# Performance work log

Measured on AMD Instinct MI355X. Metric: run time of the kernel, lower is better.

Reference implementation:

```python
import jax, jax.numpy as jnp
import numpy as np


def setup_inputs() -> dict:
    key = jax.random.key(0)
    k_x, k_g, k_fc, k_pj = jax.random.split(key, 4)
    B, T, C, H, E = 4, 2048, 1024, 2048, 8
    n_layer = 12
    x = jax.random.normal(k_x, (B, T, C), dtype=jnp.float32)
    w_gate = 0.02 * jax.random.normal(k_g, (C, E), dtype=jnp.float32)
    w_fc = 0.02 * jax.random.normal(k_fc, (C, H, E), dtype=jnp.float32)
    w_proj = (0.02 * (2 * n_layer) ** -0.5) * jax.random.normal(k_pj, (H, C, E), dtype=jnp.float32)
    return {"x": x, "w_gate": w_gate, "w_fc": w_fc, "w_proj": w_proj, "top_k": 2}


def reference(x, w_gate, w_fc, w_proj, top_k):
    # x: (B,T,C); w_gate: (C,E); w_fc: (C,H,E); w_proj: (H,C,E)
    E = w_gate.shape[-1]
    gate = jnp.einsum('btc,ce->bte', x, w_gate)                  # gating logits
    top_vals, top_idx = jax.lax.top_k(gate, top_k)               # (B,T,K) — raw logits used as combine weights (as in source)
    # Per-expert combine weight: sum_k top_val_k * onehot(idx_k) — zero for unselected experts.
    # This is mathematically identical to gathering the K expert weight slices per token
    # (the source's gather+einsum) but avoids the (B,T,C,H,K) weight blowup.
    onehot = jax.nn.one_hot(top_idx, E, dtype=x.dtype)           # (B,T,K,E)
    w_e = jnp.einsum('btk,btke->bte', top_vals, onehot)          # (B,T,E)
    h = jax.nn.silu(jnp.einsum('btc,che->bthe', x, w_fc))        # (B,T,H,E)
    o = jnp.einsum('bthe,bte,hce->btc', h, w_e, w_proj)          # weighted expert combine
    return o
```

## Files before the change

kernel.cpp:

```cpp
#include <hip/hip_runtime.h>
#include <hip/hip_bf16.h>


#define NTOK 8192
#define CD   1024
#define HD   2048
#define NE   8
#define NSLOT 16384
#define MTILES 20
#define BK   64
#define PACK_BLOCKS 2048

typedef short  short4_t  __attribute__((ext_vector_type(4)));
typedef short  short8_t  __attribute__((ext_vector_type(8)));
typedef __bf16 bf16x8_t  __attribute__((ext_vector_type(8)));
typedef float  f32x4_t   __attribute__((ext_vector_type(4)));

struct FragArg {
  short8_t v;
  __device__ operator short8_t() const { return v; }
  __device__ operator bf16x8_t() const { return __builtin_bit_cast(bf16x8_t, v); }
};

static __device__ __forceinline__ float b2f(unsigned short u) {
  union { float f; unsigned int i; } w; w.i = ((unsigned int)u) << 16; return w.f;
}
static __device__ __forceinline__ unsigned short f2b(float f) {
  unsigned int u = __float_as_uint(f);
  u += 0x7fffu + ((u >> 16) & 1u);
  return (unsigned short)(u >> 16);
}
static __device__ __forceinline__ void gl2lds16(const void* g, void* l) {
  __builtin_amdgcn_global_load_lds((__attribute__((address_space(1))) void*)g,
                                   (__attribute__((address_space(3))) void*)l,
                                   16, 0, 0);
}

static __device__ __forceinline__ void pack_tile(
    const float* __restrict__ in, unsigned short* __restrict__ out,
    int D0, int D1, int b0, int b1, unsigned short* smem, int t)
{
  int d1i = t & 31, d0q = t >> 5;
  #pragma unroll
  for (int r = 0; r < 4; ++r) {
    int d0i = d0q * 4 + r;
    const float* src = in + ((size_t)(b0 + d0i) * D1 + (b1 + d1i)) * NE;
    float4 v0 = *(const float4*)src;
    float4 v1 = *(const float4*)(src + 4);
    unsigned short* dst0 = &smem[d1i * 40 + d0i];
    dst0[0 * 32 * 40] = f2b(v0.x);
    dst0[1 * 32 * 40] = f2b(v0.y);
    dst0[2 * 32 * 40] = f2b(v0.z);
    dst0[3 * 32 * 40] = f2b(v0.w);
    dst0[4 * 32 * 40] = f2b(v1.x);
    dst0[5 * 32 * 40] = f2b(v1.y);
    dst0[6 * 32 * 40] = f2b(v1.z);
    dst0[7 * 32 * 40] = f2b(v1.w);
  }
  __syncthreads();
  int dchunk = t & 3, d1w = (t >> 2) & 31, ehalf = t >> 7;
  #pragma unroll
  for (int p = 0; p < 4; ++p) {
    int e = ehalf + 2 * p;
    short8_t v = *(const short8_t*)&smem[e * 32 * 40 + d1w * 40 + dchunk * 8];
    *(short8_t*)(out + ((size_t)e * D1 + (b1 + d1w)) * D0 + b0 + dchunk * 8) = v;
  }
}

#define GATE_BLOCKS (NTOK / 4)
__global__ __launch_bounds__(256) void prep_kernel(
    const float* __restrict__ x, const float* __restrict__ wg,
    const float* __restrict__ wfc,
    unsigned short* __restrict__ xb, unsigned short* __restrict__ wfcp,
    int* __restrict__ tok_e, float* __restrict__ tok_v,
    int* __restrict__ g_counts)
{
  __shared__ __align__(16) unsigned short lds[NE * 32 * 40];
  __shared__ int hist[NE];
  int t = threadIdx.x;

  if (blockIdx.x < GATE_BLOCKS) {
    if (t < NE) hist[t] = 0;
    __syncthreads();
    int wv = t >> 6, lane = t & 63;
    int tk = blockIdx.x * 4 + wv;
    const float* xr = x + (size_t)tk * CD;
    unsigned short* xbr = xb + (size_t)tk * CD;
    float acc[NE] = {0, 0, 0, 0, 0, 0, 0, 0};
    #pragma unroll
    for (int jj = 0; jj < 4; ++jj) {
      int c0 = (lane + 64 * jj) * 4;
      float4 xv = *(const float4*)(xr + c0);
      short4_t ob;
      ob[0] = (short)f2b(xv.x); ob[1] = (short)f2b(xv.y);
      ob[2] = (short)f2b(xv.z); ob[3] = (short)f2b(xv.w);
      *(short4_t*)(xbr + c0) = ob;
      #pragma unroll
      for (int j = 0; j < 4; ++j) {
        float xf = (j == 0) ? xv.x : (j == 1) ? xv.y : (j == 2) ? xv.z : xv.w;
        const float* wr = wg + (size_t)(c0 + j) * NE;
        float4 w0 = *(const float4*)wr;
        float4 w1 = *(const float4*)(wr + 4);
        acc[0] += xf * w0.x; acc[1] += xf * w0.y;
        acc[2] += xf * w0.z; acc[3] += xf * w0.w;
        acc[4] += xf * w1.x; acc[5] += xf * w1.y;
        acc[6] += xf * w1.z; acc[7] += xf * w1.w;
      }
    }
    #pragma unroll
    for (int off = 32; off >= 1; off >>= 1)
      #pragma unroll
      for (int e = 0; e < NE; ++e) acc[e] += __shfl_down(acc[e], off, 64);
    if (lane == 0) {
      float v1 = -3.0e38f, v2 = -3.0e38f; int i1 = 0, i2 = 1;
      #pragma unroll
      for (int e = 0; e < NE; ++e) {
        float g = acc[e];
        if (g > v1) { v2 = v1; i2 = i1; v1 = g; i1 = e; }
        else if (g > v2) { v2 = g; i2 = e; }
      }
      tok_e[tk * 2] = i1; tok_e[tk * 2 + 1] = i2;
      tok_v[tk * 2] = v1; tok_v[tk * 2 + 1] = v2;
      atomicAdd(&hist[i1], 1); atomicAdd(&hist[i2], 1);
    }
    __syncthreads();
    if (t < NE && hist[t] > 0) atomicAdd(&g_counts[t], hist[t]);
  } else {
    int pid = blockIdx.x - GATE_BLOCKS;
    int bx = pid & 63, by = pid >> 6;
    pack_tile(wfc, wfcp, CD, HD, by * 32, bx * 32, lds, t);
  }
}

__global__ __launch_bounds__(256) void scatter_kernel(
    const int* __restrict__ tok_e, const float* __restrict__ tok_v,
    const int* __restrict__ g_counts, int* __restrict__ g_cursor,
    int* __restrict__ g_base,
    int* __restrict__ bucket_tok, float* __restrict__ bucket_v,
    int* __restrict__ slot_of)
{
  int gid = blockIdx.x * 256 + threadIdx.x;
  int lane = threadIdx.x & 63;
  int base[NE];
  { int o = 0;
    #pragma unroll
    for (int e = 0; e < NE; ++e) { base[e] = o; o += g_counts[e]; } }
  int e = tok_e[gid];
  unsigned long long lanebit = 1ull << lane;
  int pos = 0;
  #pragma unroll
  for (int ee = 0; ee < NE; ++ee) {
    unsigned long long m = __ballot(e == ee);
    if (e == ee) {
      int leader = __ffsll((long long)m) - 1;
      int cnt = __popcll(m);
      int start = 0;
      if (lane == leader) start = atomicAdd(&g_cursor[ee], cnt);
      start = __shfl(start, leader, 64);
      pos = start + __popcll(m & (lanebit - 1));
    }
  }
  int sl = base[e] + pos;
  bucket_tok[sl] = gid >> 1;
  bucket_v[sl]   = tok_v[gid];
  slot_of[gid]   = sl;
  if (gid < NE) g_base[gid] = base[gid];
}

__global__ __launch_bounds__(256) void gemm1_kernel(
    const unsigned short* __restrict__ xb, const unsigned short* __restrict__ wfcp,
    const float* __restrict__ wpj, unsigned short* __restrict__ wpjp,
    const int* __restrict__ g_counts, const int* __restrict__ g_base,
    const int* __restrict__ bucket_tok, const float* __restrict__ bucket_v,
    unsigned short* __restrict__ hbuf)
{
  __shared__ __align__(16) unsigned short smem[128 * BK * 2];
  __shared__ int   s_tok[128];
  __shared__ float s_v[128];
  int t = threadIdx.x;

  if (blockIdx.x < PACK_BLOCKS) {
    int pid = blockIdx.x;
    int bx = pid & 63, by = pid >> 6;
    pack_tile(wpj, wpjp, HD, CD, bx * 32, by * 32, smem, t);
    return;
  }

  int id = blockIdx.x - PACK_BLOCKS;
  int e = id & 7;
  int r = id >> 3;
  int nt = r & 15;
  int mt = r >> 4;

  int cnt = g_counts[e];
  int m0 = mt * 128;
  if (m0 >= cnt) return;
  int base = g_base[e];
  int n0 = nt * 128;

  unsigned short* lsA = smem;
  unsigned short* lsB = smem + 128 * BK;

  if (t < 128) {
    int ok = (m0 + t) < cnt;
    s_tok[t] = ok ? bucket_tok[base + m0 + t] : 0;
    s_v[t]   = ok ? bucket_v[base + m0 + t] : 0.0f;
  }
  __syncthreads();

  int lane = t & 63, wv = t >> 6;
  int subrow = lane >> 3, kc = lane & 7;
  const unsigned short* pA[4]; const unsigned short* pB[4];
  unsigned short* dA[4]; unsigned short* dB[4];
  #pragma unroll
  for (int p = 0; p < 4; ++p) {
    int rr = p * 32 + wv * 8 + subrow;
    int gc = kc ^ ((rr >> 1) & 7);
    pA[p] = xb + (size_t)s_tok[rr] * CD + gc * 8;
    pB[p] = wfcp + ((size_t)e * HD + n0 + rr) * CD + gc * 8;
    dA[p] = &lsA[(p * 32 + wv * 8) * BK];
    dB[p] = &lsB[(p * 32 + wv * 8) * BK];
  }

  int wm = (wv & 1) * 64, wn = (wv >> 1) * 64;
  int ml = lane & 15, kq = lane >> 4;

  f32x4_t acc[4][4];
  #pragma unroll
  for (int i = 0; i < 4; ++i)
    #pragma unroll
    for (int j = 0; j < 4; ++j) acc[i][j] = (f32x4_t){0.f, 0.f, 0.f, 0.f};

  for (int k0 = 0; k0 < CD; k0 += BK) {
    __syncthreads();
    #pragma unroll
    for (int p = 0; p < 4; ++p) {
      gl2lds16(pA[p], dA[p]); pA[p] += BK;
      gl2lds16(pB[p], dB[p]); pB[p] += BK;
    }
    __syncthreads();
    #pragma unroll
    for (int s = 0; s < 2; ++s) {
      short8_t af[4], bfr[4];
      #pragma unroll
      for (int i = 0; i < 4; ++i) {
        int ar = wm + i * 16 + ml;
        af[i]  = *(const short8_t*)&lsA[ar * BK + (((s * 4 + kq) ^ ((ar >> 1) & 7)) * 8)];
        int br = wn + i * 16 + ml;
        bfr[i] = *(const short8_t*)&lsB[br * BK + (((s * 4 + kq) ^ ((br >> 1) & 7)) * 8)];
      }
      #pragma unroll
      for (int i = 0; i < 4; ++i)
        #pragma unroll
        for (int j = 0; j < 4; ++j)
          acc[i][j] = __builtin_amdgcn_mfma_f32_16x16x32_bf16(
              FragArg{af[i]}, FragArg{bfr[j]}, acc[i][j], 0, 0, 0);
    }
  }

  #pragma unroll
  for (int i = 0; i < 4; ++i) {
    int rb = wm + i * 16 + kq * 4;
    #pragma unroll
    for (int r2 = 0; r2 < 4; ++r2) {
      int row = rb + r2;
      if (m0 + row < cnt) {
        float v = s_v[row];
        size_t ro = (size_t)(base + m0 + row) * HD + n0;
        #pragma unroll
        for (int j = 0; j < 4; ++j) {
          float z = acc[i][j][r2];
          float val = v * (z / (1.0f + __expf(-z)));
          hbuf[ro + wn + j * 16 + ml] = f2b(val);
        }
      }
    }
  }
}

__global__ __launch_bounds__(256) void gemm2_kernel(
    const unsigned short* __restrict__ hbuf, const unsigned short* __restrict__ wpjp,
    const int* __restrict__ g_counts, const int* __restrict__ g_base,
    unsigned short* __restrict__ oslot)
{
  int id = blockIdx.x;
  int e = id & 7;
  int r = id >> 3;
  int nt = r & 7;
  int mt = r >> 3;

  int cnt = g_counts[e];
  int m0 = mt * 128;
  if (m0 >= cnt) return;
  int base = g_base[e];
  int n0 = nt * 128;

  __shared__ __align__(16) unsigned short lsA[128 * BK];
  __shared__ __align__(16) unsigned short lsB[128 * BK];

  int t = threadIdx.x;
  int lane = t & 63, wv = t >> 6;
  int subrow = lane >> 3, kc = lane & 7;
  const unsigned short* pA[4]; const unsigned short* pB[4];
  unsigned short* dA[4]; unsigned short* dB[4];
  #pragma unroll
  for (int p = 0; p < 4; ++p) {
    int rr = p * 32 + wv * 8 + subrow;
    int gc = kc ^ ((rr >> 1) & 7);
    pA[p] = hbuf + ((size_t)(base + m0 + rr)) * HD + gc * 8;
    pB[p] = wpjp + ((size_t)e * CD + n0 + rr) * HD + gc * 8;
    dA[p] = &lsA[(p * 32 + wv * 8) * BK];
    dB[p] = &lsB[(p * 32 + wv * 8) * BK];
  }

  int wm = (wv & 1) * 64, wn = (wv >> 1) * 64;
  int ml = lane & 15, kq = lane >> 4;

  f32x4_t acc[4][4];
  #pragma unroll
  for (int i = 0; i < 4; ++i)
    #pragma unroll
    for (int j = 0; j < 4; ++j) acc[i][j] = (f32x4_t){0.f, 0.f, 0.f, 0.f};

  for (int k0 = 0; k0 < HD; k0 += BK) {
    __syncthreads();
    #pragma unroll
    for (int p = 0; p < 4; ++p) {
      gl2lds16(pA[p], dA[p]); pA[p] += BK;
      gl2lds16(pB[p], dB[p]); pB[p] += BK;
    }
    __syncthreads();
    #pragma unroll
    for (int s = 0; s < 2; ++s) {
      short8_t af[4], bfr[4];
      #pragma unroll
      for (int i = 0; i < 4; ++i) {
        int ar = wm + i * 16 + ml;
        af[i]  = *(const short8_t*)&lsA[ar * BK + (((s * 4 + kq) ^ ((ar >> 1) & 7)) * 8)];
        int br = wn + i * 16 + ml;
        bfr[i] = *(const short8_t*)&lsB[br * BK + (((s * 4 + kq) ^ ((br >> 1) & 7)) * 8)];
      }
      #pragma unroll
      for (int i = 0; i < 4; ++i)
        #pragma unroll
        for (int j = 0; j < 4; ++j)
          acc[i][j] = __builtin_amdgcn_mfma_f32_16x16x32_bf16(
              FragArg{af[i]}, FragArg{bfr[j]}, acc[i][j], 0, 0, 0);
    }
  }

  #pragma unroll
  for (int i = 0; i < 4; ++i) {
    int rb = wm + i * 16 + kq * 4;
    #pragma unroll
    for (int r2 = 0; r2 < 4; ++r2) {
      int row = rb + r2;
      if (m0 + row < cnt) {
        size_t ro = (size_t)(base + m0 + row) * CD + n0;
        #pragma unroll
        for (int j = 0; j < 4; ++j)
          oslot[ro + wn + j * 16 + ml] = f2b(acc[i][j][r2]);
      }
    }
  }
}

__global__ __launch_bounds__(256) void combine_kernel(
    const unsigned short* __restrict__ oslot, const int* __restrict__ slot_of,
    float* __restrict__ out)
{
  int gid = blockIdx.x * 256 + threadIdx.x;
  int tk = gid >> 7;
  int ch = (gid & 127) * 8;
  int s0 = slot_of[tk * 2], s1 = slot_of[tk * 2 + 1];
  short8_t a = *(const short8_t*)(oslot + (size_t)s0 * CD + ch);
  short8_t b = *(const short8_t*)(oslot + (size_t)s1 * CD + ch);
  float* op = out + (size_t)tk * CD + ch;
  float4 o0, o1;
  o0.x = b2f((unsigned short)a[0]) + b2f((unsigned short)b[0]);
  o0.y = b2f((unsigned short)a[1]) + b2f((unsigned short)b[1]);
  o0.z = b2f((unsigned short)a[2]) + b2f((unsigned short)b[2]);
  o0.w = b2f((unsigned short)a[3]) + b2f((unsigned short)b[3]);
  o1.x = b2f((unsigned short)a[4]) + b2f((unsigned short)b[4]);
  o1.y = b2f((unsigned short)a[5]) + b2f((unsigned short)b[5]);
  o1.z = b2f((unsigned short)a[6]) + b2f((unsigned short)b[6]);
  o1.w = b2f((unsigned short)a[7]) + b2f((unsigned short)b[7]);
  *(float4*)op = o0;
  *(float4*)(op + 4) = o1;
}

extern "C" void kernel_launch(void* const* d_in, const int* in_sizes, int n_in,
                              void* d_out, int out_size, void* d_ws, size_t ws_size,
                              hipStream_t stream)
{
  const float* x   = (const float*)d_in[0];
  const float* wg  = (const float*)d_in[1];
  const float* wfc = (const float*)d_in[2];
  const float* wpj = (const float*)d_in[3];
  float* out = (float*)d_out;

  char* w = (char*)d_ws;
  unsigned short* wfcp  = (unsigned short*)w; w += (size_t)NE * HD * CD * 2;
  unsigned short* wpjp  = (unsigned short*)w; w += (size_t)NE * CD * HD * 2;
  unsigned short* xb    = (unsigned short*)w; w += (size_t)NTOK * CD * 2;
  unsigned short* hbuf  = (unsigned short*)w; w += (size_t)NSLOT * HD * 2;
  unsigned short* oslot = (unsigned short*)w; w += (size_t)NSLOT * CD * 2;
  int*   tok_e      = (int*)w;   w += NSLOT * 4;
  float* tok_v      = (float*)w; w += NSLOT * 4;
  int*   slot_of    = (int*)w;   w += NSLOT * 4;
  int*   bucket_tok = (int*)w;   w += NSLOT * 4;
  float* bucket_v   = (float*)w; w += NSLOT * 4;
  int*   g_counts   = (int*)w;   w += NE * 4;
  int*   g_cursor   = (int*)w;   w += NE * 4;
  int*   g_base     = (int*)w;   w += 256;

  hipMemsetAsync(g_counts, 0, 2 * NE * sizeof(int), stream);
  prep_kernel<<<GATE_BLOCKS + PACK_BLOCKS, 256, 0, stream>>>(
      x, wg, wfc, xb, wfcp, tok_e, tok_v, g_counts);
  scatter_kernel<<<NSLOT / 256, 256, 0, stream>>>(
      tok_e, tok_v, g_counts, g_cursor, g_base, bucket_tok, bucket_v, slot_of);
  gemm1_kernel<<<PACK_BLOCKS + (HD / 128) * MTILES * NE, 256, 0, stream>>>(
      xb, wfcp, wpj, wpjp, g_counts, g_base, bucket_tok, bucket_v, hbuf);
  gemm2_kernel<<<(CD / 128) * MTILES * NE, 256, 0, stream>>>(
      hbuf, wpjp, g_counts, g_base, oslot);
  combine_kernel<<<(NTOK * CD / 8) / 256, 256, 0, stream>>>(oslot, slot_of, out);
}
```

Before: 449.8 us.

## Double-buffer LDS with half-K staging and explicit waitcnt pipelining in expert GEMMs

Both expert GEMM kernels move from a load, sync, compute loop to a double-buffered LDS pipeline. K tiles are split into 32-wide halves, and global-to-LDS copies for later halves are issued while MFMAs run on the current half. The code uses explicit s_waitcnt vmcnt counts with raw s_barrier calls, raises wave priority around MFMA blocks, and uses a new swizzle for the 32-column layout. Launch bounds now request 2 blocks per CU. The goal is to hide global-load latency behind matrix math, at the cost of hand-counted wait logic that breaks if the number of loads per stage changes.

```diff
diff --git a/kernel.cpp b/kernel.cpp
--- a/kernel.cpp
+++ b/kernel.cpp
@@ -9,6 +9,8 @@
 #define NSLOT 16384
 #define MTILES 20
 #define BK   64
+#define NT1  (CD / BK)
+#define NT2  (HD / BK)
 #define PACK_BLOCKS 2048
 
 typedef short  short4_t  __attribute__((ext_vector_type(4)));
@@ -167,14 +169,14 @@
   if (gid < NE) g_base[gid] = base[gid];
 }
 
-__global__ __launch_bounds__(256) void gemm1_kernel(
+__global__ __launch_bounds__(256, 2) void gemm1_kernel(
     const unsigned short* __restrict__ xb, const unsigned short* __restrict__ wfcp,
     const float* __restrict__ wpj, unsigned short* __restrict__ wpjp,
     const int* __restrict__ g_counts, const int* __restrict__ g_base,
     const int* __restrict__ bucket_tok, const float* __restrict__ bucket_v,
     unsigned short* __restrict__ hbuf)
 {
-  __shared__ __align__(16) unsigned short smem[128 * BK * 2];
+  __shared__ __align__(16) unsigned short smem[2][2][2][128][32];
   __shared__ int   s_tok[128];
   __shared__ float s_v[128];
   int t = threadIdx.x;
@@ -182,7 +184,7 @@
   if (blockIdx.x < PACK_BLOCKS) {
     int pid = blockIdx.x;
     int bx = pid & 63, by = pid >> 6;
-    pack_tile(wpj, wpjp, HD, CD, bx * 32, by * 32, smem, t);
+    pack_tile(wpj, wpjp, HD, CD, bx * 32, by * 32, &smem[0][0][0][0][0], t);
     return;
   }
 
@@ -198,9 +200,6 @@
   int base = g_base[e];
   int n0 = nt * 128;
 
-  unsigned short* lsA = smem;
-  unsigned short* lsB = smem + 128 * BK;
-
   if (t < 128) {
     int ok = (m0 + t) < cnt;
     s_tok[t] = ok ? bucket_tok[base + m0 + t] : 0;
@@ -209,21 +208,26 @@
   __syncthreads();
 
   int lane = t & 63, wv = t >> 6;
-  int subrow = lane >> 3, kc = lane & 7;
-  const unsigned short* pA[4]; const unsigned short* pB[4];
-  unsigned short* dA[4]; unsigned short* dB[4];
-  #pragma unroll
-  for (int p = 0; p < 4; ++p) {
-    int rr = p * 32 + wv * 8 + subrow;
-    int gc = kc ^ ((rr >> 1) & 7);
-    pA[p] = xb + (size_t)s_tok[rr] * CD + gc * 8;
-    pB[p] = wfcp + ((size_t)e * HD + n0 + rr) * CD + gc * 8;
-    dA[p] = &lsA[(p * 32 + wv * 8) * BK];
-    dB[p] = &lsB[(p * 32 + wv * 8) * BK];
-  }
+  int srow = t >> 2;
+  int spc  = t & 3;
+  int sw   = (spc ^ (srow & 3)) * 8;
+  const unsigned short* aS0 = xb + (size_t)s_tok[srow] * CD + sw;
+  const unsigned short* aS1 = xb + (size_t)s_tok[srow + 64] * CD + sw;
+  const unsigned short* bS0 = wfcp + ((size_t)e * HD + n0 + srow) * CD + sw;
+  const unsigned short* bS1 = wfcp + ((size_t)e * HD + n0 + srow + 64) * CD + sw;
+
+  #define STG1(tt, kh) do {                                              \
+    int _ko = (tt) * BK + (kh) * 32;                                     \
+    int _b  = (tt) & 1;                                                  \
+    gl2lds16(aS0 + _ko, &smem[0][_b][kh][wv * 16][0]);                   \
+    gl2lds16(aS1 + _ko, &smem[0][_b][kh][64 + wv * 16][0]);              \
+    gl2lds16(bS0 + _ko, &smem[1][_b][kh][wv * 16][0]);                   \
+    gl2lds16(bS1 + _ko, &smem[1][_b][kh][64 + wv * 16][0]);              \
+  } while (0)
 
   int wm = (wv & 1) * 64, wn = (wv >> 1) * 64;
   int ml = lane & 15, kq = lane >> 4;
+  int sw8 = (kq ^ (ml & 3)) * 8;
 
   f32x4_t acc[4][4];
   #pragma unroll
@@ -231,32 +235,55 @@
     #pragma unroll
     for (int j = 0; j < 4; ++j) acc[i][j] = (f32x4_t){0.f, 0.f, 0.f, 0.f};
 
-  for (int k0 = 0; k0 < CD; k0 += BK) {
-    __syncthreads();
-    #pragma unroll
-    for (int p = 0; p < 4; ++p) {
-      gl2lds16(pA[p], dA[p]); pA[p] += BK;
-      gl2lds16(pB[p], dB[p]); pB[p] += BK;
-    }
-    __syncthreads();
-    #pragma unroll
-    for (int s = 0; s < 2; ++s) {
-      short8_t af[4], bfr[4];
-      #pragma unroll
-      for (int i = 0; i < 4; ++i) {
-        int ar = wm + i * 16 + ml;
-        af[i]  = *(const short8_t*)&lsA[ar * BK + (((s * 4 + kq) ^ ((ar >> 1) & 7)) * 8)];
-        int br = wn + i * 16 + ml;
-        bfr[i] = *(const short8_t*)&lsB[br * BK + (((s * 4 + kq) ^ ((br >> 1) & 7)) * 8)];
-      }
-      #pragma unroll
-      for (int i = 0; i < 4; ++i)
-        #pragma unroll
-        for (int j = 0; j < 4; ++j)
-          acc[i][j] = __builtin_amdgcn_mfma_f32_16x16x32_bf16(
-              FragArg{af[i]}, FragArg{bfr[j]}, acc[i][j], 0, 0, 0);
-    }
-  }
+  STG1(0, 0); STG1(0, 1); STG1(1, 0);
+  asm volatile("s_waitcnt vmcnt(8)" ::: "memory");
+  __builtin_amdgcn_s_barrier();
+  asm volatile("" ::: "memory");
+
+  #pragma unroll 1
+  for (int tt = 0; tt < NT1; ++tt) {
+    int buf = tt & 1;
+    short8_t af[4], bfr[4];
+    #pragma unroll
+    for (int i = 0; i < 4; ++i) {
+      af[i]  = *(const short8_t*)&smem[0][buf][0][wm + i * 16 + ml][sw8];
+      bfr[i] = *(const short8_t*)&smem[1][buf][0][wn + i * 16 + ml][sw8];
+    }
+    if (tt + 1 < NT1) STG1(tt + 1, 1);
+    __builtin_amdgcn_s_barrier();
+    __builtin_amdgcn_s_setprio(1);
+    #pragma unroll
+    for (int i = 0; i < 4; ++i)
+      #pragma unroll
+      for (int j = 0; j < 4; ++j)
+        acc[i][j] = __builtin_amdgcn_mfma_f32_16x16x32_bf16(
+            FragArg{af[i]}, FragArg{bfr[j]}, acc[i][j], 0, 0, 0);
+    __builtin_amdgcn_s_setprio(0);
+    if (tt < NT1 - 1) asm volatile("s_waitcnt vmcnt(8)" ::: "memory");
+    else              asm volatile("s_waitcnt vmcnt(0)" ::: "memory");
+    __builtin_amdgcn_s_barrier();
+    asm volatile("" ::: "memory");
+    #pragma unroll
+    for (int i = 0; i < 4; ++i) {
+      af[i]  = *(const short8_t*)&smem[0][buf][1][wm + i * 16 + ml][sw8];
+      bfr[i] = *(const short8_t*)&smem[1][buf][1][wn + i * 16 + ml][sw8];
+    }
+    if (tt + 2 < NT1) STG1(tt + 2, 0);
+    __builtin_amdgcn_s_barrier();
+    __builtin_amdgcn_s_setprio(1);
+    #pragma unroll
+    for (int i = 0; i < 4; ++i)
+      #pragma unroll
+      for (int j = 0; j < 4; ++j)
+        acc[i][j] = __builtin_amdgcn_mfma_f32_16x16x32_bf16(
+            FragArg{af[i]}, FragArg{bfr[j]}, acc[i][j], 0, 0, 0);
+    __builtin_amdgcn_s_setprio(0);
+    if (tt + 2 < NT1)      asm volatile("s_waitcnt vmcnt(8)" ::: "memory");
+    else if (tt + 1 < NT1) asm volatile("s_waitcnt vmcnt(4)" ::: "memory");
+    __builtin_amdgcn_s_barrier();
+    asm volatile("" ::: "memory");
+  }
+  #undef STG1
 
   #pragma unroll
   for (int i = 0; i < 4; ++i) {
@@ -278,11 +305,13 @@
   }
 }
 
-__global__ __launch_bounds__(256) void gemm2_kernel(
+__global__ __launch_bounds__(256, 2) void gemm2_kernel(
     const unsigned short* __restrict__ hbuf, const unsigned short* __restrict__ wpjp,
     const int* __restrict__ g_counts, const int* __restrict__ g_base,
     unsigned short* __restrict__ oslot)
 {
+  __shared__ __align__(16) unsigned short smem[2][2][2][128][32];
+
   int id = blockIdx.x;
   int e = id & 7;
   int r = id >> 3;
@@ -295,26 +324,28 @@
   int base = g_base[e];
   int n0 = nt * 128;
 
-  __shared__ __align__(16) unsigned short lsA[128 * BK];
-  __shared__ __align__(16) unsigned short lsB[128 * BK];
-
   int t = threadIdx.x;
   int lane = t & 63, wv = t >> 6;
-  int subrow = lane >> 3, kc = lane & 7;
-  const unsigned short* pA[4]; const unsigned short* pB[4];
-  unsigned short* dA[4]; unsigned short* dB[4];
-  #pragma unroll
-  for (int p = 0; p < 4; ++p) {
-    int rr = p * 32 + wv * 8 + subrow;
-    int gc = kc ^ ((rr >> 1) & 7);
-    pA[p] = hbuf + ((size_t)(base + m0 + rr)) * HD + gc * 8;
-    pB[p] = wpjp + ((size_t)e * CD + n0 + rr) * HD + gc * 8;
-    dA[p] = &lsA[(p * 32 + wv * 8) * BK];
-    dB[p] = &lsB[(p * 32 + wv * 8) * BK];
-  }
+  int srow = t >> 2;
+  int spc  = t & 3;
+  int sw   = (spc ^ (srow & 3)) * 8;
+  const unsigned short* aS0 = hbuf + ((size_t)(base + m0 + srow)) * HD + sw;
+  const unsigned short* aS1 = hbuf + ((size_t)(base + m0 + srow + 64)) * HD + sw;
+  const unsigned short* bS0 = wpjp + ((size_t)e * CD + n0 + srow) * HD + sw;
+  const unsigned short* bS1 = wpjp + ((size_t)e * CD + n0 + srow + 64) * HD + sw;
+
+  #define STG2(tt, kh) do {                                              \
+    int _ko = (tt) * BK + (kh) * 32;                                     \
+    int _b  = (tt) & 1;                                                  \
+    gl2lds16(aS0 + _ko, &smem[0][_b][kh][wv * 16][0]);                   \
+    gl2lds16(aS1 + _ko, &smem[0][_b][kh][64 + wv * 16][0]);              \
+    gl2lds16(bS0 + _ko, &smem[1][_b][kh][wv * 16][0]);                   \
+    gl2lds16(bS1 + _ko, &smem[1][_b][kh][64 + wv * 16][0]);              \
+  } while (0)
 
   int wm = (wv & 1) * 64, wn = (wv >> 1) * 64;
   int ml = lane & 15, kq = lane >> 4;
+  int sw8 = (kq ^ (ml & 3)) * 8;
 
   f32x4_t acc[4][4];
   #pragma unroll
@@ -322,32 +353,56 @@
     #pragma unroll
     for (int j = 0; j < 4; ++j) acc[i][j] = (f32x4_t){0.f, 0.f, 0.f, 0.f};
 
-  for (int k0 = 0; k0 < HD; k0 += BK) {
-    __syncthreads();
-    #pragma unroll
-    for (int p = 0; p < 4; ++p) {
-      gl2lds16(pA[p], dA[p]); pA[p] += BK;
-      gl2lds16(pB[p], dB[p]); pB[p] += BK;
-    }
-    __syncthreads();
-    #pragma unroll
-    for (int s = 0; s < 2; ++s) {
-      short8_t af[4], bfr[4];
-      #pragma unroll
-      for (int i = 0; i < 4; ++i) {
-        int ar = wm + i * 16 + ml;
-        af[i]  = *(const short8_t*)&lsA[ar * BK + (((s * 4 + kq) ^ ((ar >> 1) & 7)) * 8)];
-        int br = wn + i * 16 + ml;
-        bfr[i] = *(const short8_t*)&lsB[br * BK + (((s * 4 + kq) ^ ((br >> 1) & 7)) * 8)];
-      }
-      #pragma unroll
-      for (int i = 0; i < 4; ++i)
-        #pragma unroll
-        for (int j = 0; j < 4; ++j)
-          acc[i][j] = __builtin_amdgcn_mfma_f32_16x16x32_bf16(
-              FragArg{af[i]}, FragArg{bfr[j]}, acc[i][j], 0, 0, 0);
-    }
-  }
+  asm volatile("s_waitcnt vmcnt(0)" ::: "memory");
+  STG2(0, 0); STG2(0, 1); STG2(1, 0);
+  asm volatile("s_waitcnt vmcnt(8)" ::: "memory");
+  __builtin_amdgcn_s_barrier();
+  asm volatile("" ::: "memory");
+
+  #pragma unroll 1
+  for (int tt = 0; tt < NT2; ++tt) {
+    int buf = tt & 1;
+    short8_t af[4], bfr[4];
+    #pragma unroll
+    for (int i = 0; i < 4; ++i) {
+      af[i]  = *(const short8_t*)&smem[0][buf][0][wm + i * 16 + ml][sw8];
+      bfr[i] = *(const short8_t*)&smem[1][buf][0][wn + i * 16 + ml][sw8];
+    }
+    if (tt + 1 < NT2) STG2(tt + 1, 1);
+    __builtin_amdgcn_s_barrier();
+    __builtin_amdgcn_s_setprio(1);
+    #pragma unroll
+    for (int i = 0; i < 4; ++i)
+      #pragma unroll
+      for (int j = 0; j < 4; ++j)
+        acc[i][j] = __builtin_amdgcn_mfma_f32_16x16x32_bf16(
+            FragArg{af[i]}, FragArg{bfr[j]}, acc[i][j], 0, 0, 0);
+    __builtin_amdgcn_s_setprio(0);
+    if (tt < NT2 - 1) asm volatile("s_waitcnt vmcnt(8)" ::: "memory");
+    else              asm volatile("s_waitcnt vmcnt(0)" ::: "memory");
+    __builtin_amdgcn_s_barrier();
+    asm volatile("" ::: "memory");
+    #pragma unroll
+    for (int i = 0; i < 4; ++i) {
+      af[i]  = *(const short8_t*)&smem[0][buf][1][wm + i * 16 + ml][sw8];
+      bfr[i] = *(const short8_t*)&smem[1][buf][1][wn + i * 16 + ml][sw8];
+    }
+    if (tt + 2 < NT2) STG2(tt + 2, 0);
+    __builtin_amdgcn_s_barrier();
+    __builtin_amdgcn_s_setprio(1);
+    #pragma unroll
+    for (int i = 0; i < 4; ++i)
+      #pragma unroll
+      for (int j = 0; j < 4; ++j)
+        acc[i][j] = __builtin_amdgcn_mfma_f32_16x16x32_bf16(
+            FragArg{af[i]}, FragArg{bfr[j]}, acc[i][j], 0, 0, 0);
+    __builtin_amdgcn_s_setprio(0);
+    if (tt + 2 < NT2)      asm volatile("s_waitcnt vmcnt(8)" ::: "memory");
+    else if (tt + 1 < NT2) asm volatile("s_waitcnt vmcnt(4)" ::: "memory");
+    __builtin_amdgcn_s_barrier();
+    asm volatile("" ::: "memory");
+  }
+  #undef STG2
 
   #pragma unroll
   for (int i = 0; i < 4; ++i) {
```

After: 447.0 us. About the same (-0.6%).
